# Optimization experiments

Measured on AMD Instinct MI355X. Metric: run time of the kernel, lower is better.

Reference implementation:

```python
import jax, jax.numpy as jnp
import numpy as np

KNN_K = 8
WINDOW = 3  # temporal_window + 1 candidate frames
LN_EPS = 1e-5
NORM_EPS = 1e-12


def setup_inputs() -> dict:
    key = jax.random.key(0)
    B, T, M, D, H = 2, 8, 512, 1024, 1024
    ks = jax.random.split(key, 12)
    s = 0.02
    return {
        "z": jax.random.normal(ks[0], (B, T, M, D), jnp.float32),
        "Wq": jax.random.normal(ks[1], (D, D), jnp.float32) * s,
        "Wv": jax.random.normal(ks[2], (D, D), jnp.float32) * s,
        "Wout": jax.random.normal(ks[3], (D, D), jnp.float32) * s,
        "ln_w": jnp.ones((D,), jnp.float32),
        "ln_b": jnp.zeros((D,), jnp.float32),
        "Watt_q": jax.random.normal(ks[4], (D, D), jnp.float32) * s,
        "Watt_k": jax.random.normal(ks[5], (D, D), jnp.float32) * s,
        "W_ih": jax.random.normal(ks[6], (3 * H, D), jnp.float32) * s,
        "W_hh": jax.random.normal(ks[7], (3 * H, H), jnp.float32) * s,
        "b_ih": jnp.zeros((3 * H,), jnp.float32),
        "b_hh": jnp.zeros((3 * H,), jnp.float32),
        "W_mf": jax.random.normal(ks[8], (D, H), jnp.float32) * s,
        "b_mf": jnp.zeros((D,), jnp.float32),
    }


def _forward(z, Wq, Wv, Wout, ln_w, ln_b, Watt_q, Watt_k,
             W_ih, W_hh, b_ih, b_hh, W_mf, b_mf):
    B, T, M, D = z.shape
    H = W_hh.shape[1]
    # cosine normalization (torch F.normalize with eps clamp)
    zn = z / jnp.maximum(jnp.linalg.norm(z, axis=-1, keepdims=True), NORM_EPS)
    mem = jnp.zeros((B, M, H), z.dtype)
    b_ar = jnp.arange(B)[:, None, None]
    outs = []
    for t in range(T):  # T is static; fully vectorized over B, M, k inside
        tts = t - jnp.arange(WINDOW)          # candidate frames t, t-1, t-2
        valid = tts >= 0                      # [W]
        cand = zn[:, jnp.clip(tts, 0)]        # [B,W,M,D]
        # cosine similarity query nodes at t vs all candidates (dt-major order)
        sim = jnp.einsum('bmd,bwnd->bmwn', zn[:, t], cand).reshape(B, M, WINDOW * M)
        sim = jnp.where(jnp.repeat(valid, M)[None, None, :], sim, -jnp.inf)
        vals, idx = jax.lax.top_k(sim, KNN_K)  # [B,M,k]
        dt = idx // M
        j = idx % M
        tt = jnp.clip(t - dt, 0)
        Kfeat = z[b_ar, tt, j]                 # [B,M,k,D] gathered neighbors
        # GAT quirk faithful to source: scalar logit scale from node 0's query,
        # first output coordinate only, shared across all nodes of (b,t)
        s0 = z[:, t, 0] @ Watt_q[0]            # [B]
        kh_sum = (Kfeat @ Watt_k.T).sum(-1)    # [B,M,k]
        att = jax.nn.softmax(s0[:, None, None] * kh_sum, axis=-1)
        alpha = 0.5 * vals + 0.5 * att         # [B,M,k]
        msg = jnp.einsum('bmk,bmkd->bmd', alpha, Kfeat @ Wv.T)
        h_t = z[:, t]                          # [B,M,D]
        x = msg + h_t @ Wq.T
        mu = x.mean(-1, keepdims=True)
        var = ((x - mu) ** 2).mean(-1, keepdims=True)
        x = (x - mu) / jnp.sqrt(var + LN_EPS) * ln_w + ln_b
        inp = x @ Wout.T
        # torch GRUCell: gates ordered (r, z, n)
        gi = inp @ W_ih.T + b_ih               # [B,M,3H]
        gh = mem @ W_hh.T + b_hh
        ir, iz, inn = jnp.split(gi, 3, axis=-1)
        hr, hz, hn = jnp.split(gh, 3, axis=-1)
        r = jax.nn.sigmoid(ir + hr)
        zg = jax.nn.sigmoid(iz + hz)
        n = jnp.tanh(inn + r * hn)
        mem = (1.0 - zg) * n + zg * mem
        outs.append(h_t + mem @ W_mf.T + b_mf)
    h = jnp.stack(outs, axis=1)                # [B,T,M,D]
    return h, mem


def reference(z, Wq, Wv, Wout, ln_w, ln_b, Watt_q, Watt_k,
              W_ih, W_hh, b_ih, b_hh, W_mf, b_mf):
    return _forward(z, Wq, Wv, Wout, ln_w, ln_b, Watt_q, Watt_k,
                    W_ih, W_hh, b_ih, b_hh, W_mf, b_mf)
```

## Files before the change

### kernel.cpp

```cpp
#include <hip/hip_runtime.h>
#include <hip/hip_bf16.h>
#include <math.h>

#define B_ 2
#define T_ 8
#define M_ 512
#define D_ 1024
#define H_ 1024
#define NC_ 1536
#define KNN 8

typedef __hip_bfloat16 bf16;
typedef short v8s __attribute__((ext_vector_type(8)));
typedef float v4f __attribute__((ext_vector_type(4)));

__device__ __forceinline__ float b2f(short s) {
  union { unsigned u; float f; } x; x.u = ((unsigned)(unsigned short)s) << 16; return x.f;
}
__device__ __forceinline__ short f2b(float f) {
  bf16 h = __float2bfloat16(f); return *(short*)&h;
}

__device__ __forceinline__ void async16(const void* g, void* l) {
  __builtin_amdgcn_global_load_lds(
      (const __attribute__((address_space(1))) void*)g,
      (__attribute__((address_space(3))) void*)l, 16, 0, 0);
}

__device__ __forceinline__ void mfma_loop(const bf16* __restrict__ A,
                                          const bf16* __restrict__ Bp,
                                          int K, v4f (&acc)[4][4],
                                          bf16* sA, bf16* sB)
{
  const int tid  = threadIdx.x;
  const int lane = tid & 63;
  const int wave = tid >> 6;
  const int quad = lane >> 4;
  const int l15  = lane & 15;
  const int wr = (wave >> 1) * 64;
  const int wc = (wave & 1) * 64;

  const int r0 = tid >> 2, g0 = (tid & 3) ^ ((r0 >> 1) & 3);
  const int c1 = tid + 256;
  const int r1 = c1 >> 2,  g1 = (c1 & 3) ^ ((r1 >> 1) & 3);

  const bf16* a0p = A  + (size_t)r0*K + g0*8;
  const bf16* a1p = A  + (size_t)r1*K + g1*8;
  const bf16* b0p = Bp + (size_t)r0*K + g0*8;
  const bf16* b1p = Bp + (size_t)r1*K + g1*8;
  bf16* la0 = sA + tid*8;  bf16* la1 = sA + c1*8;
  bf16* lb0 = sB + tid*8;  bf16* lb1 = sB + c1*8;

  int aoff[4], boff[4];
  #pragma unroll
  for (int i = 0; i < 4; ++i) {
    int ra = wr + i*16 + l15;
    aoff[i] = (ra*4 + (quad ^ ((ra >> 1) & 3))) * 8;
    int rb = wc + i*16 + l15;
    boff[i] = (rb*4 + (quad ^ ((rb >> 1) & 3))) * 8;
  }

  for (int k0 = 0; k0 < K; k0 += 32) {
    __syncthreads();
    async16(a0p + k0, la0);
    async16(a1p + k0, la1);
    async16(b0p + k0, lb0);
    async16(b1p + k0, lb1);
    __syncthreads();
    v8s af[4], bfr[4];
    #pragma unroll
    for (int i = 0; i < 4; ++i) af[i]  = *(const v8s*)(sA + aoff[i]);
    #pragma unroll
    for (int i = 0; i < 4; ++i) bfr[i] = *(const v8s*)(sB + boff[i]);
    #pragma unroll
    for (int mi = 0; mi < 4; ++mi)
      #pragma unroll
      for (int ni = 0; ni < 4; ++ni)
        acc[mi][ni] = __builtin_amdgcn_mfma_f32_16x16x32_bf16(
            af[mi], bfr[ni], acc[mi][ni], 0, 0, 0);
  }
}

template<bool DUAL, bool HASBIAS, bool HASADD, bool OUTBF, bool STATS>
__global__ __launch_bounds__(256) void k_bgemm(
    const bf16* __restrict__ A1, const bf16* __restrict__ B1,
    const bf16* __restrict__ A2, const bf16* __restrict__ B2,
    const float* __restrict__ bias, const float* __restrict__ add,
    void* __restrict__ Cv, int N, int K,
    float* __restrict__ ssum, float* __restrict__ ssq)
{
  __shared__ bf16 sA[128*32];
  __shared__ bf16 sB[128*32];
  v4f acc[4][4];
  #pragma unroll
  for (int i = 0; i < 4; ++i)
    #pragma unroll
    for (int j = 0; j < 4; ++j) acc[i][j] = (v4f){0.f,0.f,0.f,0.f};

  const int row0 = blockIdx.y * 128, col0 = blockIdx.x * 128;
  mfma_loop(A1 + (size_t)row0*K, B1 + (size_t)col0*K, K, acc, sA, sB);
  if constexpr (DUAL)
    mfma_loop(A2 + (size_t)row0*K, B2 + (size_t)col0*K, K, acc, sA, sB);

  const int tid = threadIdx.x, lane = tid & 63, wave = tid >> 6;
  const int quad = lane >> 4, l15 = lane & 15;
  const int wr = (wave >> 1) * 64, wc = (wave & 1) * 64;

  float st_s[4][4], st_q[4][4];
  if constexpr (STATS) {
    #pragma unroll
    for (int a = 0; a < 4; ++a)
      #pragma unroll
      for (int b = 0; b < 4; ++b) { st_s[a][b] = 0.f; st_q[a][b] = 0.f; }
  }

  #pragma unroll
  for (int ni = 0; ni < 4; ++ni) {
    const int col = col0 + wc + ni*16 + l15;
    float bv = 0.f;
    if constexpr (HASBIAS) bv = bias[col];
    #pragma unroll
    for (int mi = 0; mi < 4; ++mi) {
      const int rowb = row0 + wr + mi*16 + quad*4;
      #pragma unroll
      for (int reg = 0; reg < 4; ++reg) {
        const int row = rowb + reg;
        float v = acc[mi][ni][reg] + bv;
        if constexpr (HASADD) v += add[(size_t)row*N + col];
        if constexpr (STATS) { st_s[mi][reg] += v; st_q[mi][reg] += v*v; }
        if constexpr (OUTBF)
          ((bf16*)Cv)[(size_t)row*N + col] = __float2bfloat16(v);
        else
          ((float*)Cv)[(size_t)row*N + col] = v;
      }
    }
  }

  if constexpr (STATS) {
    const int p = blockIdx.x*2 + (wave & 1);
    #pragma unroll
    for (int mi = 0; mi < 4; ++mi)
      #pragma unroll
      for (int reg = 0; reg < 4; ++reg) {
        float s = st_s[mi][reg], q = st_q[mi][reg];
        #pragma unroll
        for (int o = 1; o < 16; o <<= 1) {
          s += __shfl_xor(s, o, 64);
          q += __shfl_xor(q, o, 64);
        }
        if (l15 == 0) {
          const int row = row0 + wr + mi*16 + quad*4 + reg;
          ssum[(size_t)p*8192 + row] = s;
          ssq [(size_t)p*8192 + row] = q;
        }
      }
  }
}

__global__ __launch_bounds__(256) void k_inp(
    const bf16* __restrict__ Xb, const bf16* __restrict__ Bw,
    const float* __restrict__ ssum, const float* __restrict__ ssq,
    const float* __restrict__ u, const float* __restrict__ vv,
    bf16* __restrict__ Cv)
{
  __shared__ bf16 sA[128*32];
  __shared__ bf16 sB[128*32];
  __shared__ float smu[128], srs[128];
  const int row0 = blockIdx.y * 128, col0 = blockIdx.x * 128;
  const int tid = threadIdx.x;
  if (tid < 128) {
    int r = row0 + tid;
    float s = 0.f, q = 0.f;
    #pragma unroll
    for (int p = 0; p < 16; ++p) { s += ssum[(size_t)p*8192 + r]; q += ssq[(size_t)p*8192 + r]; }
    float mu = s * (1.f/D_);
    float var = q * (1.f/D_) - mu*mu;
    smu[tid] = mu; srs[tid] = rsqrtf(var + 1e-5f);
  }
  __syncthreads();

  v4f acc[4][4];
  #pragma unroll
  for (int i = 0; i < 4; ++i)
    #pragma unroll
    for (int j = 0; j < 4; ++j) acc[i][j] = (v4f){0.f,0.f,0.f,0.f};
  mfma_loop(Xb + (size_t)row0*D_, Bw + (size_t)col0*D_, D_, acc, sA, sB);

  const int lane = tid & 63, wave = tid >> 6;
  const int quad = lane >> 4, l15 = lane & 15;
  const int wr = (wave >> 1) * 64, wc = (wave & 1) * 64;
  #pragma unroll
  for (int ni = 0; ni < 4; ++ni) {
    const int col = col0 + wc + ni*16 + l15;
    const float uj = u[col], vj = vv[col];
    #pragma unroll
    for (int mi = 0; mi < 4; ++mi) {
      const int rl = wr + mi*16 + quad*4;
      #pragma unroll
      for (int reg = 0; reg < 4; ++reg) {
        const float mu = smu[rl+reg], rs = srs[rl+reg];
        float v = rs*acc[mi][ni][reg] - mu*rs*uj + vj;
        Cv[(size_t)(row0+rl+reg)*D_ + col] = __float2bfloat16(v);
      }
    }
  }
}

__global__ __launch_bounds__(256) void k_sims(const bf16* __restrict__ znhi,
                                              const bf16* __restrict__ znlo,
                                              const float* __restrict__ z,
                                              const float* __restrict__ wks,
                                              float* __restrict__ sim,
                                              float* __restrict__ kh)
{
  __shared__ bf16 sAh[128*32];
  __shared__ bf16 sAl[128*32];
  __shared__ bf16 sBh[128*32];
  __shared__ bf16 sBl[128*32];

  const int zi = blockIdx.z;
  const int tid  = threadIdx.x;
  const int lane = tid & 63;
  const int wave = tid >> 6;

  if (zi >= 48) {
    int kid = (zi - 48)*16 + blockIdx.y*4 + blockIdx.x;
    int r = kid*4 + wave;
    const float* zp = z + (size_t)r*D_ + lane*16;
    const float* wp = wks + lane*16;
    float p = 0.f;
    #pragma unroll
    for (int j = 0; j < 4; ++j) {
      float4 a = *(const float4*)(zp + j*4);
      float4 b = *(const float4*)(wp + j*4);
      p += a.x*b.x + a.y*b.y + a.z*b.z + a.w*b.w;
    }
    for (int o = 32; o; o >>= 1) p += __shfl_down(p, o, 64);
    if (lane == 0) kh[r] = p;
    return;
  }

  const int w  = zi % 3;
  const int bt = zi / 3;
  const int b  = bt / T_;
  const int t  = bt % T_;
  if (w > t) return;
  const int tw = t - w;
  const int arow0 = bt*M_ + blockIdx.y*128;
  const int brow0 = (b*T_ + tw)*M_ + blockIdx.x*128;

  const bf16* Ah = znhi + (size_t)arow0*D_;
  const bf16* Al = znlo + (size_t)arow0*D_;
  const bf16* Bh = znhi + (size_t)brow0*D_;
  const bf16* Bl = znlo + (size_t)brow0*D_;

  v4f acc[4][4];
  #pragma unroll
  for (int i = 0; i < 4; ++i)
    #pragma unroll
    for (int j = 0; j < 4; ++j) acc[i][j] = (v4f){0.f,0.f,0.f,0.f};

  const int quad = lane >> 4;
  const int l15  = lane & 15;
  const int wr = (wave >> 1) * 64;
  const int wc = (wave & 1) * 64;

  const int r0 = tid >> 2, g0 = (tid & 3) ^ ((r0 >> 1) & 3);
  const int c1 = tid + 256;
  const int r1 = c1 >> 2,  g1 = (c1 & 3) ^ ((r1 >> 1) & 3);
  const size_t o0 = (size_t)r0*D_ + g0*8;
  const size_t o1 = (size_t)r1*D_ + g1*8;

  int aoff[4], boff[4];
  #pragma unroll
  for (int i = 0; i < 4; ++i) {
    int ra = wr + i*16 + l15;
    aoff[i] = (ra*4 + (quad ^ ((ra >> 1) & 3))) * 8;
    int rb = wc + i*16 + l15;
    boff[i] = (rb*4 + (quad ^ ((rb >> 1) & 3))) * 8;
  }

  for (int k0 = 0; k0 < D_; k0 += 32) {
    __syncthreads();
    async16(Ah + o0 + k0, sAh + tid*8);
    async16(Ah + o1 + k0, sAh + c1*8);
    async16(Al + o0 + k0, sAl + tid*8);
    async16(Al + o1 + k0, sAl + c1*8);
    async16(Bh + o0 + k0, sBh + tid*8);
    async16(Bh + o1 + k0, sBh + c1*8);
    async16(Bl + o0 + k0, sBl + tid*8);
    async16(Bl + o1 + k0, sBl + c1*8);
    __syncthreads();
    v8s ah[4], al[4], bh[4], bl[4];
    #pragma unroll
    for (int i = 0; i < 4; ++i) {
      ah[i] = *(const v8s*)(sAh + aoff[i]);
      al[i] = *(const v8s*)(sAl + aoff[i]);
      bh[i] = *(const v8s*)(sBh + boff[i]);
      bl[i] = *(const v8s*)(sBl + boff[i]);
    }
    #pragma unroll
    for (int mi = 0; mi < 4; ++mi)
      #pragma unroll
      for (int ni = 0; ni < 4; ++ni) {
        acc[mi][ni] = __builtin_amdgcn_mfma_f32_16x16x32_bf16(ah[mi], bh[ni], acc[mi][ni], 0, 0, 0);
        acc[mi][ni] = __builtin_amdgcn_mfma_f32_16x16x32_bf16(ah[mi], bl[ni], acc[mi][ni], 0, 0, 0);
        acc[mi][ni] = __builtin_amdgcn_mfma_f32_16x16x32_bf16(al[mi], bh[ni], acc[mi][ni], 0, 0, 0);
      }
  }

  float* C = sim + (size_t)bt*M_*NC_;
  const int rowbase = blockIdx.y*128 + wr;
  const int colbase = w*M_ + blockIdx.x*128 + wc;
  #pragma unroll
  for (int ni = 0; ni < 4; ++ni) {
    const int col = colbase + ni*16 + l15;
    #pragma unroll
    for (int mi = 0; mi < 4; ++mi) {
      const int rowb = rowbase + mi*16 + quad*4;
      #pragma unroll
      for (int reg = 0; reg < 4; ++reg)
        C[(size_t)(rowb+reg)*NC_ + col] = acc[mi][ni][reg];
    }
  }
}

__global__ __launch_bounds__(256) void k_fgru2(
    const bf16* __restrict__ membIn, const bf16* __restrict__ Whhb,
    const bf16* __restrict__ gib, const float* __restrict__ b_hh,
    float* __restrict__ mem, bf16* __restrict__ membOut,
    bf16* __restrict__ memhb, float* __restrict__ outT, int t)
{
  __shared__ bf16 sA[64*32];
  __shared__ bf16 sB[3][64*32];

  const int row0 = blockIdx.y*64, col0 = blockIdx.x*64;

  const int tid  = threadIdx.x;
  const int lane = tid & 63;
  const int wave = tid >> 6;
  const int quad = lane >> 4;
  const int l15  = lane & 15;
  const int wr   = (wave >> 1) * 32;
  const int wcol = (wave & 1) * 32;

  const int rA = tid >> 2, gA = (tid & 3) ^ ((rA >> 1) & 3);
  const size_t aofs = (size_t)rA*H_ + gA*8;
  const size_t bofs = (size_t)(col0 + rA)*H_ + gA*8;

  int aoff[2], boff[2];
  #pragma unroll
  for (int i = 0; i < 2; ++i) {
    int ra = wr + i*16 + l15;
    aoff[i] = (ra*4 + (quad ^ ((ra >> 1) & 3))) * 8;
    int rb = wcol + i*16 + l15;
    boff[i] = (rb*4 + (quad ^ ((rb >> 1) & 3))) * 8;
  }

  v4f acc[3][2][2];
  #pragma unroll
  for (int g = 0; g < 3; ++g)
    #pragma unroll
    for (int i = 0; i < 2; ++i)
      #pragma unroll
      for (int j = 0; j < 2; ++j) acc[g][i][j] = (v4f){0.f,0.f,0.f,0.f};

  if (t > 0) {
    const bf16* prev = membIn + (size_t)row0*H_;
    for (int k0 = 0; k0 < H_; k0 += 32) {
      __syncthreads();
      async16(prev + aofs + k0, sA + tid*8);
      async16(Whhb + bofs + k0,           sB[0] + tid*8);
      async16(Whhb + 1048576 + bofs + k0, sB[1] + tid*8);
      async16(Whhb + 2097152 + bofs + k0, sB[2] + tid*8);
      __syncthreads();
      v8s af[2], bfr[3][2];
      #pragma unroll
      for (int i = 0; i < 2; ++i) af[i] = *(const v8s*)(sA + aoff[i]);
      #pragma unroll
      for (int g = 0; g < 3; ++g)
        #pragma unroll
        for (int i = 0; i < 2; ++i) bfr[g][i] = *(const v8s*)(sB[g] + boff[i]);
      #pragma unroll
      for (int g = 0; g < 3; ++g)
        #pragma unroll
        for (int mi = 0; mi < 2; ++mi)
          #pragma unroll
          for (int ni = 0; ni < 2; ++ni)
            acc[g][mi][ni] = __builtin_amdgcn_mfma_f32_16x16x32_bf16(
                af[mi], bfr[g][ni], acc[g][mi][ni], 0, 0, 0);
    }
  }

  #pragma unroll
  for (int ni = 0; ni < 2; ++ni) {
    const int col = col0 + wcol + ni*16 + l15;
    const float bhr = b_hh[col];
    const float bhz = b_hh[H_ + col];
    const float bhn = b_hh[2*H_ + col];
    #pragma unroll
    for (int mi = 0; mi < 2; ++mi) {
      const int rowb = row0 + wr + mi*16 + quad*4;
      #pragma unroll
      for (int reg = 0; reg < 4; ++reg) {
        const int row = rowb + reg;
        const int b = row >> 9, m = row & 511;
        const size_t btm = (size_t)((b*T_ + t)*M_ + m);
        const bf16* gp = gib + btm*(3*H_);
        float ir  = b2f(*(const short*)(gp + col));
        float iz  = b2f(*(const short*)(gp + H_ + col));
        float inn = b2f(*(const short*)(gp + 2*H_ + col));
        float hr = acc[0][mi][ni][reg] + bhr;
        float hz = acc[1][mi][ni][reg] + bhz;
        float hn = acc[2][mi][ni][reg] + bhn;
        float rgt = 1.f/(1.f + expf(-(ir + hr)));
        float zgt = 1.f/(1.f + expf(-(iz + hz)));
        float n   = tanhf(inn + rgt*hn);
        const size_t mo = (size_t)row*H_ + col;
        float mold = (t > 0) ? mem[mo] : 0.f;
        float mnew = (1.f - zgt)*n + zgt*mold;
        mem[mo] = mnew;
        bf16 mb = __float2bfloat16(mnew);
        membOut[mo] = mb;
        memhb[btm*H_ + col] = mb;
        if (t == T_-1) outT[mo] = mnew;
      }
    }
  }
}

__global__ __launch_bounds__(256) void k_prep(
    const float* __restrict__ Wq, const float* __restrict__ Wv,
    const float* __restrict__ Wout, const float* __restrict__ Wih,
    const float* __restrict__ Whh, const float* __restrict__ Wmf,
    const float* __restrict__ lnw, const float* __restrict__ lnb,
    const float* __restrict__ Wattk, const float* __restrict__ Wattq,
    const float* __restrict__ z,
    bf16* __restrict__ Wdst, float* __restrict__ wks,
    float* __restrict__ u, float* __restrict__ vv, float* __restrict__ s0,
    bf16* __restrict__ zb, bf16* __restrict__ znhi, bf16* __restrict__ znlo)
{
  __shared__ float ps[4], pk[4];
  const int bid = blockIdx.x, tid = threadIdx.x;

  if (bid < 10240) {
    int i = bid*256 + tid;
    const float* src; int base;
    if      (i <  262144) { src = Wq;   base = 0; }
    else if (i <  524288) { src = Wv;   base = 262144; }
    else if (i <  786432) { src = Wout; base = 524288; }
    else if (i < 1572864) { src = Wih;  base = 786432; }
    else if (i < 2359296) { src = Whh;  base = 1572864; }
    else                  { src = Wmf;  base = 2359296; }
    float4 v = ((const float4*)src)[i - base];
    if (i >= 524288 && i < 786432) {
      int d = (i*4) & 1023;
      float4 w = *(const float4*)(lnw + d);
      v.x *= w.x; v.y *= w.y; v.z *= w.z; v.w *= w.w;
    }
    *(short4*)(Wdst + (size_t)i*4) = make_short4(f2b(v.x), f2b(v.y), f2b(v.z), f2b(v.w));
  } else if (bid < 10368) {
    int rc = bid - 10240;
    int rowc = rc >> 2, colc = rc & 3;
    int d = colc*256 + tid;
    float s = 0.f;
    for (int r = rowc*32; r < rowc*32 + 32; ++r) s += Wattk[(size_t)r*D_ + d];
    atomicAdd(&wks[d], s);
  } else if (bid < 10624) {
    int j = (bid - 10368)*4 + (tid >> 6);
    int l = tid & 63;
    const float* wr_ = Wout + (size_t)j*D_ + l*16;
    const float* aw = lnw + l*16;
    const float* ab = lnb + l*16;
    float pu = 0.f, pv = 0.f;
    #pragma unroll
    for (int q = 0; q < 4; ++q) {
      float4 a = *(const float4*)(wr_ + q*4);
      float4 x = *(const float4*)(aw + q*4);
      float4 y = *(const float4*)(ab + q*4);
      pu += a.x*x.x + a.y*x.y + a.z*x.z + a.w*x.w;
      pv += a.x*y.x + a.y*y.y + a.z*y.z + a.w*y.w;
    }
    for (int o = 32; o; o >>= 1) { pu += __shfl_down(pu, o, 64); pv += __shfl_down(pv, o, 64); }
    if (l == 0) { u[j] = pu; vv[j] = pv; }
  } else if (bid < 10640) {
    int bt = bid - 10624;
    int d = tid*4;
    float4 a = *(const float4*)(z + (size_t)bt*M_*D_ + d);
    float4 q = *(const float4*)(Wattq + d);
    float p = a.x*q.x + a.y*q.y + a.z*q.z + a.w*q.w;
    for (int o = 32; o; o >>= 1) p += __shfl_down(p, o, 64);
    if ((tid & 63) == 0) ps[tid >> 6] = p;
    __syncthreads();
    if (tid == 0) s0[bt] = ps[0]+ps[1]+ps[2]+ps[3];
  } else {
    int row = bid - 10640;
    const float* zr = z + (size_t)row*D_;
    int d = tid*4;
    float4 v = *(const float4*)(zr + d);
    float ss = v.x*v.x + v.y*v.y + v.z*v.z + v.w*v.w;
    for (int o = 32; o; o >>= 1) ss += __shfl_down(ss, o, 64);
    if ((tid & 63) == 0) pk[tid >> 6] = ss;
    __syncthreads();
    float s = pk[0]+pk[1]+pk[2]+pk[3];
    float rn = 1.0f / fmaxf(sqrtf(s), 1e-12f);
    *(short4*)(zb + (size_t)row*D_ + d) = make_short4(f2b(v.x), f2b(v.y), f2b(v.z), f2b(v.w));
    float zn[4] = {v.x*rn, v.y*rn, v.z*rn, v.w*rn};
    short hi[4], lo[4];
    #pragma unroll
    for (int j = 0; j < 4; ++j) {
      hi[j] = f2b(zn[j]);
      lo[j] = f2b(zn[j] - b2f(hi[j]));
    }
    *(short4*)(znhi + (size_t)row*D_ + d) = make_short4(hi[0],hi[1],hi[2],hi[3]);
    *(short4*)(znlo + (size_t)row*D_ + d) = make_short4(lo[0],lo[1],lo[2],lo[3]);
  }
}

__global__ __launch_bounds__(256) void k_topk(
    const float* __restrict__ sim, const float* __restrict__ kh,
    const float* __restrict__ s0, const bf16* __restrict__ zb,
    bf16* __restrict__ kbarb)
{
  const int wave = threadIdx.x >> 6, l = threadIdx.x & 63;
  const int r  = blockIdx.x*4 + wave;
  const int bt = r >> 9, m = r & 511;
  const int b  = bt >> 3, t = bt & 7;
  const float* srow = sim + (size_t)bt*M_*NC_ + (size_t)m*NC_;
  const int limit = (t >= 2) ? NC_ : ((t == 1) ? 2*M_ : M_);

  float v[24];
  #pragma unroll
  for (int j = 0; j < 24; ++j) {
    int i = j*64 + l;
    v[j] = (i < limit) ? srow[i] : -INFINITY;
  }

  float selv[KNN]; int seli[KNN];
  #pragma unroll
  for (int k = 0; k < KNN; ++k) {
    float bv = v[0]; int bj = 0;
    #pragma unroll
    for (int j = 1; j < 24; ++j)
      if (v[j] > bv) { bv = v[j]; bj = j; }
    int bi = bj*64 + l;
    #pragma unroll
    for (int o = 1; o < 64; o <<= 1) {
      float ov = __shfl_xor(bv, o, 64);
      int   oi = __shfl_xor(bi, o, 64);
      if (ov > bv || (ov == bv && oi < bi)) { bv = ov; bi = oi; }
    }
    selv[k] = bv; seli[k] = bi;
    if ((bi & 63) == l) {
      int jj = bi >> 6;
      #pragma unroll
      for (int j = 0; j < 24; ++j) if (j == jj) v[j] = -INFINITY;
    }
  }

  float khv = 0.f;
  if (l < KNN) {
    int idx = seli[l];
    int w = idx >> 9, n = idx & 511;
    int tt = t - w;
    khv = kh[(b*T_ + tt)*M_ + n];
  }
  float s0v = s0[bt];
  float att[KNN], mx = -INFINITY;
  #pragma unroll
  for (int k = 0; k < KNN; ++k) { att[k] = s0v * __shfl(khv, k, 64); mx = fmaxf(mx, att[k]); }
  float den = 0.f;
  #pragma unroll
  for (int k = 0; k < KNN; ++k) { att[k] = expf(att[k]-mx); den += att[k]; }
  float rden = 1.0f/den;
  float alpha[KNN];
  #pragma unroll
  for (int k = 0; k < KNN; ++k) alpha[k] = 0.5f*selv[k] + 0.5f*att[k]*rden;

  const int d0 = l*16;
  float o[16];
  #pragma unroll
  for (int e = 0; e < 16; ++e) o[e] = 0.f;
  #pragma unroll
  for (int k = 0; k < KNN; ++k) {
    int idx = seli[k];
    int w = idx >> 9, n = idx & 511;
    int tt = t - w;
    const bf16* zp = zb + ((size_t)((b*T_ + tt)*M_ + n))*D_ + d0;
    v8s z0 = *(const v8s*)zp;
    v8s z1 = *(const v8s*)(zp + 8);
    float al = alpha[k];
    #pragma unroll
    for (int e = 0; e < 8; ++e) {
      o[e]   = fmaf(al, b2f(z0[e]), o[e]);
      o[8+e] = fmaf(al, b2f(z1[e]), o[8+e]);
    }
  }
  bf16* kp = kbarb + (size_t)r*D_ + d0;
  short outv[16];
  #pragma unroll
  for (int e = 0; e < 16; ++e) outv[e] = f2b(o[e]);
  *(v8s*)kp       = *(v8s*)outv;
  *(v8s*)(kp + 8) = *(v8s*)(outv + 8);
}

extern "C" void kernel_launch(void* const* d_in, const int* in_sizes, int n_in,
                              void* d_out, int out_size, void* d_ws, size_t ws_size,
                              hipStream_t stream) {
  (void)in_sizes; (void)n_in; (void)out_size; (void)ws_size;
  const float* z      = (const float*)d_in[0];
  const float* Wq     = (const float*)d_in[1];
  const float* Wv     = (const float*)d_in[2];
  const float* Wout   = (const float*)d_in[3];
  const float* ln_w   = (const float*)d_in[4];
  const float* ln_b   = (const float*)d_in[5];
  const float* Watt_q = (const float*)d_in[6];
  const float* Watt_k = (const float*)d_in[7];
  const float* W_ih   = (const float*)d_in[8];
  const float* W_hh   = (const float*)d_in[9];
  const float* b_ih   = (const float*)d_in[10];
  const float* b_hh   = (const float*)d_in[11];
  const float* W_mf   = (const float*)d_in[12];
  const float* b_mf   = (const float*)d_in[13];
  float* out = (float*)d_out;
  float* ws  = (float*)d_ws;

  float* sim   = ws;
  bf16*  GIb   = (bf16*)ws;
  bf16*  znhi  = (bf16*)(ws + 12582912);
  bf16*  Xb    = znhi;
  bf16*  zb    = (bf16*)(ws + 16777216);
  bf16*  kbarb = (bf16*)(ws + 20971520);
  bf16*  INPb  = kbarb;
  bf16*  memhb = (bf16*)(ws + 25165824);
  bf16*  znlo  = memhb;
  bf16*  mA    = (bf16*)(ws + 29360128);
  bf16*  mB    = (bf16*)(ws + 29884416);
  float* mem   = ws + 30408704;
  bf16*  Wqb   = (bf16*)(ws + 31457280);
  bf16*  Wvb   = Wqb + 1048576;
  bf16*  Woutb = Wqb + 2097152;
  bf16*  Wihb  = Wqb + 3145728;
  bf16*  Whhb  = Wqb + 6291456;
  bf16*  Wmfb  = Wqb + 9437184;
  float* wks   = ws + 36700160;
  float* s0    = ws + 36701184;
  float* kh    = ws + 36701200;
  float* u     = ws + 36709392;
  float* vv    = ws + 36710416;
  float* ssum  = ws + 36711440;
  float* ssq   = ws + 36842512;

  hipMemsetAsync(wks, 0, 1024*sizeof(float), stream);

  k_prep<<<dim3(18832), dim3(256), 0, stream>>>(
      Wq, Wv, Wout, W_ih, W_hh, W_mf, ln_w, ln_b, Watt_k, Watt_q, z,
      Wqb, wks, u, vv, s0, zb, znhi, znlo);

  k_sims<<<dim3(4,4,176), dim3(256), 0, stream>>>(znhi, znlo, z, wks, sim, kh);

  k_topk<<<dim3(2048), dim3(256), 0, stream>>>(sim, kh, s0, zb, kbarb);

  k_bgemm<true,false,false,true,true><<<dim3(8,64), dim3(256), 0, stream>>>(
      kbarb, Wvb, zb, Wqb, nullptr, nullptr, Xb, D_, D_, ssum, ssq);

  k_inp<<<dim3(8,64), dim3(256), 0, stream>>>(Xb, Woutb, ssum, ssq, u, vv, INPb);

  k_bgemm<false,true,false,true,false><<<dim3(24,64), dim3(256), 0, stream>>>(
      INPb, Wihb, nullptr, nullptr, b_ih, nullptr, GIb, 3*H_, D_, nullptr, nullptr);

  for (int t = 0; t < T_; ++t) {
    bf16*       mout = (t & 1) ? mB : mA;
    const bf16* min_ = (t & 1) ? mA : mB;
    k_fgru2<<<dim3(16,16), dim3(256), 0, stream>>>(
        min_, Whhb, GIb, b_hh, mem, mout, memhb,
        out + (size_t)B_*T_*M_*D_, t);
  }

  k_bgemm<false,true,true,false,false><<<dim3(8,64), dim3(256), 0, stream>>>(
      memhb, Wmfb, nullptr, nullptr, b_mf, z, out, D_, H_, nullptr, nullptr);
}
```

Measured before the change: 671.1 us.

## Fold Wout into W_ih weights and overlap output GEMM with GRU steps

```diff
diff --git a/kernel.cpp b/kernel.cpp
--- a/kernel.cpp
+++ b/kernel.cpp
@@ -81,12 +81,43 @@
   }
 }
 
-template<bool DUAL, bool HASBIAS, bool HASADD, bool OUTBF, bool STATS>
+__device__ __forceinline__ void out_tile(int oid, int tp,
+    const bf16* __restrict__ memhb, const bf16* __restrict__ Wmfb,
+    const float* __restrict__ b_mf, const float* __restrict__ z,
+    float* __restrict__ out, bf16* sA, bf16* sB)
+{
+  const int rb = oid >> 3, cb = oid & 7;
+  const int g0 = (rb >> 2)*4096 + tp*512 + (rb & 3)*128;
+  v4f acc[4][4];
+  #pragma unroll
+  for (int i = 0; i < 4; ++i)
+    #pragma unroll
+    for (int j = 0; j < 4; ++j) acc[i][j] = (v4f){0.f,0.f,0.f,0.f};
+  mfma_loop(memhb + (size_t)g0*H_, Wmfb + (size_t)(cb*128)*H_, H_, acc, sA, sB);
+  const int tid = threadIdx.x, lane = tid & 63, wave = tid >> 6;
+  const int quad = lane >> 4, l15 = lane & 15;
+  const int wr = (wave >> 1) * 64, wcc = (wave & 1) * 64;
+  #pragma unroll
+  for (int ni = 0; ni < 4; ++ni) {
+    const int col = cb*128 + wcc + ni*16 + l15;
+    const float bv = b_mf[col];
+    #pragma unroll
+    for (int mi = 0; mi < 4; ++mi) {
+      const int rowb = g0 + wr + mi*16 + quad*4;
+      #pragma unroll
+      for (int reg = 0; reg < 4; ++reg) {
+        const int row = rowb + reg;
+        out[(size_t)row*D_ + col] = acc[mi][ni][reg] + bv + z[(size_t)row*D_ + col];
+      }
+    }
+  }
+}
+
+template<bool DUAL, bool STATS>
 __global__ __launch_bounds__(256) void k_bgemm(
     const bf16* __restrict__ A1, const bf16* __restrict__ B1,
     const bf16* __restrict__ A2, const bf16* __restrict__ B2,
-    const float* __restrict__ bias, const float* __restrict__ add,
-    void* __restrict__ Cv, int N, int K,
+    bf16* __restrict__ Cv, int N, int K,
     float* __restrict__ ssum, float* __restrict__ ssq)
 {
   __shared__ bf16 sA[128*32];
@@ -117,21 +148,14 @@
   #pragma unroll
   for (int ni = 0; ni < 4; ++ni) {
     const int col = col0 + wc + ni*16 + l15;
-    float bv = 0.f;
-    if constexpr (HASBIAS) bv = bias[col];
     #pragma unroll
     for (int mi = 0; mi < 4; ++mi) {
       const int rowb = row0 + wr + mi*16 + quad*4;
       #pragma unroll
       for (int reg = 0; reg < 4; ++reg) {
-        const int row = rowb + reg;
-        float v = acc[mi][ni][reg] + bv;
-        if constexpr (HASADD) v += add[(size_t)row*N + col];
+        float v = acc[mi][ni][reg];
         if constexpr (STATS) { st_s[mi][reg] += v; st_q[mi][reg] += v*v; }
-        if constexpr (OUTBF)
-          ((bf16*)Cv)[(size_t)row*N + col] = __float2bfloat16(v);
-        else
-          ((float*)Cv)[(size_t)row*N + col] = v;
+        Cv[(size_t)(rowb+reg)*N + col] = __float2bfloat16(v);
       }
     }
   }
@@ -157,10 +181,10 @@
   }
 }
 
-__global__ __launch_bounds__(256) void k_inp(
-    const bf16* __restrict__ Xb, const bf16* __restrict__ Bw,
+__global__ __launch_bounds__(256) void k_gic(
+    const bf16* __restrict__ Xb, const bf16* __restrict__ Wcb,
     const float* __restrict__ ssum, const float* __restrict__ ssq,
-    const float* __restrict__ u, const float* __restrict__ vv,
+    const float* __restrict__ u2, const float* __restrict__ v2b,
     bf16* __restrict__ Cv)
 {
   __shared__ bf16 sA[128*32];
@@ -184,7 +208,7 @@
   for (int i = 0; i < 4; ++i)
     #pragma unroll
     for (int j = 0; j < 4; ++j) acc[i][j] = (v4f){0.f,0.f,0.f,0.f};
-  mfma_loop(Xb + (size_t)row0*D_, Bw + (size_t)col0*D_, D_, acc, sA, sB);
+  mfma_loop(Xb + (size_t)row0*D_, Wcb + (size_t)col0*D_, D_, acc, sA, sB);
 
   const int lane = tid & 63, wave = tid >> 6;
   const int quad = lane >> 4, l15 = lane & 15;
@@ -192,7 +216,7 @@
   #pragma unroll
   for (int ni = 0; ni < 4; ++ni) {
     const int col = col0 + wc + ni*16 + l15;
-    const float uj = u[col], vj = vv[col];
+    const float uj = u2[col], vj = v2b[col];
     #pragma unroll
     for (int mi = 0; mi < 4; ++mi) {
       const int rl = wr + mi*16 + quad*4;
@@ -200,7 +224,7 @@
       for (int reg = 0; reg < 4; ++reg) {
         const float mu = smu[rl+reg], rs = srs[rl+reg];
         float v = rs*acc[mi][ni][reg] - mu*rs*uj + vj;
-        Cv[(size_t)(row0+rl+reg)*D_ + col] = __float2bfloat16(v);
+        Cv[(size_t)(row0+rl+reg)*(3*H_) + col] = __float2bfloat16(v);
       }
     }
   }
@@ -211,7 +235,16 @@
                                               const float* __restrict__ z,
                                               const float* __restrict__ wks,
                                               float* __restrict__ sim,
-                                              float* __restrict__ kh)
+                                              float* __restrict__ kh,
+                                              const bf16* __restrict__ Wihb,
+                                              const float* __restrict__ Wout,
+                                              const float* __restrict__ lnw,
+                                              const float* __restrict__ u,
+                                              const float* __restrict__ vv,
+                                              const float* __restrict__ b_ih,
+                                              bf16* __restrict__ Wcb,
+                                              float* __restrict__ u2,
+                                              float* __restrict__ v2b)
 {
   __shared__ bf16 sAh[128*32];
   __shared__ bf16 sAl[128*32];
@@ -222,6 +255,100 @@
   const int tid  = threadIdx.x;
   const int lane = tid & 63;
   const int wave = tid >> 6;
+
+  if (zi >= 176) {
+    const int slot = (zi - 176)*16 + blockIdx.y*4 + blockIdx.x;
+    if (slot < 192) {
+      const int yc = slot >> 3, xc = slot & 7;
+      const int quad = lane >> 4, l15 = lane & 15;
+      const int wr = (wave >> 1) * 64, wcc = (wave & 1) * 64;
+
+      v4f acc[4][4];
+      #pragma unroll
+      for (int i = 0; i < 4; ++i)
+        #pragma unroll
+        for (int j = 0; j < 4; ++j) acc[i][j] = (v4f){0.f,0.f,0.f,0.f};
+
+      const int r0 = tid >> 2, g0c = (tid & 3) ^ ((r0 >> 1) & 3);
+      const int c1 = tid + 256, r1 = c1 >> 2, g1c = (c1 & 3) ^ ((r1 >> 1) & 3);
+      const bf16* Ap = Wihb + (size_t)(yc*128)*D_;
+      const size_t ao0 = (size_t)r0*D_ + g0c*8;
+      const size_t ao1 = (size_t)r1*D_ + g1c*8;
+
+      const int cB = tid >> 3;
+      const int jg = (tid & 7) * 16;
+      float lw[16];
+      #pragma unroll
+      for (int e = 0; e < 16; ++e) lw[e] = lnw[xc*128 + jg + e];
+
+      int aoff[4], boff[4];
+      #pragma unroll
+      for (int i = 0; i < 4; ++i) {
+        int ra = wr + i*16 + l15;
+        aoff[i] = (ra*4 + (quad ^ ((ra >> 1) & 3))) * 8;
+        int rb = wcc + i*16 + l15;
+        boff[i] = (rb*4 + (quad ^ ((rb >> 1) & 3))) * 8;
+      }
+
+      for (int k0 = 0; k0 < D_; k0 += 32) {
+        __syncthreads();
+        async16(Ap + ao0 + k0, sAh + tid*8);
+        async16(Ap + ao1 + k0, sAh + c1*8);
+        const float* wsrc = Wout + (size_t)(k0 + cB)*D_ + xc*128 + jg;
+        #pragma unroll
+        for (int e4 = 0; e4 < 4; ++e4) {
+          float4 wv = *(const float4*)(wsrc + e4*4);
+          float vals[4] = {wv.x, wv.y, wv.z, wv.w};
+          #pragma unroll
+          for (int e = 0; e < 4; ++e) {
+            int j = jg + e4*4 + e;
+            int sl = (cB >> 3) ^ ((j >> 1) & 3);
+            sBh[(j*4 + sl)*8 + (cB & 7)] = __float2bfloat16(vals[e]*lw[e4*4+e]);
+          }
+        }
+        __syncthreads();
+        v8s af[4], bfr[4];
+        #pragma unroll
+        for (int i = 0; i < 4; ++i) af[i]  = *(const v8s*)(sAh + aoff[i]);
+        #pragma unroll
+        for (int i = 0; i < 4; ++i) bfr[i] = *(const v8s*)(sBh + boff[i]);
+        #pragma unroll
+        for (int mi = 0; mi < 4; ++mi)
+          #pragma unroll
+          for (int ni = 0; ni < 4; ++ni)
+            acc[mi][ni] = __builtin_amdgcn_mfma_f32_16x16x32_bf16(
+                af[mi], bfr[ni], acc[mi][ni], 0, 0, 0);
+      }
+      #pragma unroll
+      for (int ni = 0; ni < 4; ++ni) {
+        const int col = xc*128 + wcc + ni*16 + l15;
+        #pragma unroll
+        for (int mi = 0; mi < 4; ++mi) {
+          const int rowb = yc*128 + wr + mi*16 + quad*4;
+          #pragma unroll
+          for (int reg = 0; reg < 4; ++reg)
+            Wcb[(size_t)(rowb+reg)*D_ + col] = __float2bfloat16(acc[mi][ni][reg]);
+        }
+      }
+    } else {
+      int g = (slot - 192)*256 + tid;
+      if (g < 3*H_) {
+        const bf16* wr_ = Wihb + (size_t)g*D_;
+        float du = 0.f, dv = 0.f;
+        for (int k = 0; k < 128; ++k) {
+          v8s wv = *(const v8s*)(wr_ + k*8);
+          #pragma unroll
+          for (int e = 0; e < 8; ++e) {
+            float wf = b2f(wv[e]);
+            du += wf * u[k*8+e];
+            dv += wf * vv[k*8+e];
+          }
+        }
+        u2[g] = du; v2b[g] = dv + b_ih[g];
+      }
+    }
+    return;
+  }
 
   if (zi >= 48) {
     int kid = (zi - 48)*16 + blockIdx.y*4 + blockIdx.x;
@@ -232,8 +359,8 @@
     #pragma unroll
     for (int j = 0; j < 4; ++j) {
       float4 a = *(const float4*)(zp + j*4);
-      float4 b = *(const float4*)(wp + j*4);
-      p += a.x*b.x + a.y*b.y + a.z*b.z + a.w*b.w;
+      float b4v[4] = {wp[j*4], wp[j*4+1], wp[j*4+2], wp[j*4+3]};
+      p += a.x*b4v[0] + a.y*b4v[1] + a.z*b4v[2] + a.w*b4v[3];
     }
     for (int o = 32; o; o >>= 1) p += __shfl_down(p, o, 64);
     if (lane == 0) kh[r] = p;
@@ -329,11 +456,19 @@
     const bf16* __restrict__ membIn, const bf16* __restrict__ Whhb,
     const bf16* __restrict__ gib, const float* __restrict__ b_hh,
     float* __restrict__ mem, bf16* __restrict__ membOut,
-    bf16* __restrict__ memhb, float* __restrict__ outT, int t)
+    bf16* __restrict__ memhb, float* __restrict__ outT,
+    const bf16* __restrict__ Wmfb, const float* __restrict__ b_mf,
+    const float* __restrict__ z, float* __restrict__ outMain, int t)
 {
-  __shared__ bf16 sA[64*32];
-  __shared__ bf16 sB[3][64*32];
-
+  __shared__ bf16 smem[8192];
+
+  if (blockIdx.y >= 16) {
+    out_tile((blockIdx.y-16)*16 + blockIdx.x, t-1,
+             memhb, Wmfb, b_mf, z, outMain, smem, smem + 4096);
+    return;
+  }
+
+  bf16* sA = smem;
   const int row0 = blockIdx.y*64, col0 = blockIdx.x*64;
 
   const int tid  = threadIdx.x;
@@ -370,9 +505,9 @@
     for (int k0 = 0; k0 < H_; k0 += 32) {
       __syncthreads();
       async16(prev + aofs + k0, sA + tid*8);
-      async16(Whhb + bofs + k0,           sB[0] + tid*8);
-      async16(Whhb + 1048576 + bofs + k0, sB[1] + tid*8);
-      async16(Whhb + 2097152 + bofs + k0, sB[2] + tid*8);
+      async16(Whhb + bofs + k0,           smem + 2048 + tid*8);
+      async16(Whhb + 1048576 + bofs + k0, smem + 4096 + tid*8);
+      async16(Whhb + 2097152 + bofs + k0, smem + 6144 + tid*8);
       __syncthreads();
       v8s af[2], bfr[3][2];
       #pragma unroll
@@ -380,7 +515,8 @@
       #pragma unroll
       for (int g = 0; g < 3; ++g)
         #pragma unroll
-        for (int i = 0; i < 2; ++i) bfr[g][i] = *(const v8s*)(sB[g] + boff[i]);
+        for (int i = 0; i < 2; ++i)
+          bfr[g][i] = *(const v8s*)(smem + 2048 + g*2048 + boff[i]);
       #pragma unroll
       for (int g = 0; g < 3; ++g)
         #pragma unroll
@@ -429,6 +565,16 @@
   }
 }
 
+__global__ __launch_bounds__(256) void k_outtail(
+    const bf16* __restrict__ memhb, const bf16* __restrict__ Wmfb,
+    const float* __restrict__ b_mf, const float* __restrict__ z,
+    float* __restrict__ outMain)
+{
+  __shared__ bf16 smem[8192];
+  out_tile(blockIdx.y*8 + blockIdx.x, T_-1, memhb, Wmfb, b_mf, z, outMain,
+           smem, smem + 4096);
+}
+
 __global__ __launch_bounds__(256) void k_prep(
     const float* __restrict__ Wq, const float* __restrict__ Wv,
     const float* __restrict__ Wout, const float* __restrict__ Wih,
@@ -453,11 +599,6 @@
     else if (i < 2359296) { src = Whh;  base = 1572864; }
     else                  { src = Wmf;  base = 2359296; }
     float4 v = ((const float4*)src)[i - base];
-    if (i >= 524288 && i < 786432) {
-      int d = (i*4) & 1023;
-      float4 w = *(const float4*)(lnw + d);
-      v.x *= w.x; v.y *= w.y; v.z *= w.z; v.w *= w.w;
-    }
     *(short4*)(Wdst + (size_t)i*4) = make_short4(f2b(v.x), f2b(v.y), f2b(v.z), f2b(v.w));
   } else if (bid < 10368) {
     int rc = bid - 10240;
@@ -631,7 +772,6 @@
   bf16*  Xb    = znhi;
   bf16*  zb    = (bf16*)(ws + 16777216);
   bf16*  kbarb = (bf16*)(ws + 20971520);
-  bf16*  INPb  = kbarb;
   bf16*  memhb = (bf16*)(ws + 25165824);
   bf16*  znlo  = memhb;
   bf16*  mA    = (bf16*)(ws + 29360128);
@@ -639,7 +779,6 @@
   float* mem   = ws + 30408704;
   bf16*  Wqb   = (bf16*)(ws + 31457280);
   bf16*  Wvb   = Wqb + 1048576;
-  bf16*  Woutb = Wqb + 2097152;
   bf16*  Wihb  = Wqb + 3145728;
   bf16*  Whhb  = Wqb + 6291456;
   bf16*  Wmfb  = Wqb + 9437184;
@@ -650,6 +789,9 @@
   float* vv    = ws + 36710416;
   float* ssum  = ws + 36711440;
   float* ssq   = ws + 36842512;
+  float* u2    = ws + 36973584;
+  float* v2b   = ws + 36976656;
+  bf16*  Wcb   = (bf16*)(ws + 36979728);
 
   hipMemsetAsync(wks, 0, 1024*sizeof(float), stream);
 
@@ -657,26 +799,25 @@
       Wq, Wv, Wout, W_ih, W_hh, W_mf, ln_w, ln_b, Watt_k, Watt_q, z,
       Wqb, wks, u, vv, s0, zb, znhi, znlo);
 
-  k_sims<<<dim3(4,4,176), dim3(256), 0, stream>>>(znhi, znlo, z, wks, sim, kh);
+  k_sims<<<dim3(4,4,189), dim3(256), 0, stream>>>(
+      znhi, znlo, z, wks, sim, kh,
+      Wihb, Wout, ln_w, u, vv, b_ih, Wcb, u2, v2b);
 
   k_topk<<<dim3(2048), dim3(256), 0, stream>>>(sim, kh, s0, zb, kbarb);
 
-  k_bgemm<true,false,false,true,true><<<dim3(8,64), dim3(256), 0, stream>>>(
-      kbarb, Wvb, zb, Wqb, nullptr, nullptr, Xb, D_, D_, ssum, ssq);
-
-  k_inp<<<dim3(8,64), dim3(256), 0, stream>>>(Xb, Woutb, ssum, ssq, u, vv, INPb);
-
-  k_bgemm<false,true,false,true,false><<<dim3(24,64), dim3(256), 0, stream>>>(
-      INPb, Wihb, nullptr, nullptr, b_ih, nullptr, GIb, 3*H_, D_, nullptr, nullptr);
+  k_bgemm<true,true><<<dim3(8,64), dim3(256), 0, stream>>>(
+      kbarb, Wvb, zb, Wqb, Xb, D_, D_, ssum, ssq);
+
+  k_gic<<<dim3(24,64), dim3(256), 0, stream>>>(Xb, Wcb, ssum, ssq, u2, v2b, GIb);
 
   for (int t = 0; t < T_; ++t) {
     bf16*       mout = (t & 1) ? mB : mA;
     const bf16* min_ = (t & 1) ? mA : mB;
-    k_fgru2<<<dim3(16,16), dim3(256), 0, stream>>>(
+    dim3 grid = (t == 0) ? dim3(16,16) : dim3(16,20);
+    k_fgru2<<<grid, dim3(256), 0, stream>>>(
         min_, Whhb, GIb, b_hh, mem, mout, memhb,
-        out + (size_t)B_*T_*M_*D_, t);
-  }
-
-  k_bgemm<false,true,true,false,false><<<dim3(8,64), dim3(256), 0, stream>>>(
-      memhb, Wmfb, nullptr, nullptr, b_mf, z, out, D_, H_, nullptr, nullptr);
-}
+        out + (size_t)B_*T_*M_*D_, Wmfb, b_mf, z, out, t);
+  }
+
+  k_outtail<<<dim3(8,8), dim3(256), 0, stream>>>(memhb, Wmfb, b_mf, z, out);
+}
```

After: 686.1 us. 2.2% more time.
